# Performance work log

Hardware: AMD Instinct MI355X
Metric: run time of the kernel (lower is better)

The kernel has to match this reference:

```python
import jax, jax.numpy as jnp
import numpy as np

HIDDEN = 1024
HEADS = 16
HEAD_DIM = HIDDEN // HEADS


def setup_inputs() -> dict:
    key = jax.random.key(0)
    ks = jax.random.split(key, 9)
    s = 1.0 / np.sqrt(HIDDEN)
    inp = {
        "x": jax.random.normal(ks[0], (2, 2048, HIDDEN), dtype=jnp.float32),
        "Wq": jax.random.uniform(ks[1], (HIDDEN, HIDDEN), jnp.float32, -s, s),
        "bq": jax.random.uniform(ks[2], (HIDDEN,), jnp.float32, -s, s),
        "Wk": jax.random.uniform(ks[3], (HIDDEN, HIDDEN), jnp.float32, -s, s),
        "bk": jax.random.uniform(ks[4], (HIDDEN,), jnp.float32, -s, s),
        "Wv": jax.random.uniform(ks[5], (HIDDEN, HIDDEN), jnp.float32, -s, s),
        "bv": jax.random.uniform(ks[6], (HIDDEN,), jnp.float32, -s, s),
        "Wo": jax.random.uniform(ks[7], (HIDDEN, HIDDEN), jnp.float32, -s, s),
        "bo": jax.random.uniform(ks[8], (HIDDEN,), jnp.float32, -s, s),
    }
    return inp


def reference(x, Wq, bq, Wk, bk, Wv, bv, Wo, bo):
    B, S, _ = x.shape
    # QKV projections; reshape to [B, H, S, D]
    def heads(t):
        return t.reshape(B, S, HEADS, HEAD_DIM).transpose(0, 2, 1, 3)
    q = heads(x @ Wq + bq)
    k = heads(x @ Wk + bk)
    v = heads(x @ Wv + bv)
    scale = 1.0 / np.sqrt(HEAD_DIM)
    scores = jnp.einsum('bhqd,bhkd->bhqk', q, k) * scale  # [B,H,S,S]
    attn = jax.nn.softmax(scores, axis=-1)
    out = jnp.einsum('bhqk,bhkd->bhqd', attn, v)  # [B,H,S,D]
    out = out.transpose(0, 2, 1, 3).reshape(B, S, HIDDEN)
    return out @ Wo + bo
```

## Files before the change

kernel.cpp:

```cpp
#include <hip/hip_runtime.h>
#include <math.h>


namespace {

constexpr int kHID = 1024;
constexpr int kNH  = 16;
constexpr int kHD  = 64;
constexpr int kSEQ = 2048;

constexpr float kQScale = 0.125f * 1.4426950408889634f;

typedef unsigned short ushortT;
typedef __attribute__((ext_vector_type(8))) short   bf16x8;
typedef __attribute__((ext_vector_type(4))) float   f32x4;
typedef __attribute__((ext_vector_type(4))) unsigned short u16x4;

#define MFMA(a, b, c) __builtin_amdgcn_mfma_f32_16x16x32_bf16((a), (b), (c), 0, 0, 0)
#define SBAR() __builtin_amdgcn_s_barrier()
#define WAITV0() asm volatile("s_waitcnt vmcnt(0)" ::: "memory")
#define WAITV4() asm volatile("s_waitcnt vmcnt(4)" ::: "memory")
#define WAITV8() asm volatile("s_waitcnt vmcnt(8)" ::: "memory")

typedef const __attribute__((address_space(1))) void GVoid;
typedef __attribute__((address_space(3))) void SVoid;

__device__ __forceinline__ void gload_lds16(const ushortT* g, ushortT* l) {
    __builtin_amdgcn_global_load_lds((GVoid*)g, (SVoid*)l, 16, 0, 0);
}

__device__ __forceinline__ ushortT f2bf(float f) {
    unsigned u = __builtin_bit_cast(unsigned, f);
    u += 0x7fffu + ((u >> 16) & 1u);
    return (ushortT)(u >> 16);
}

__device__ __forceinline__ unsigned cvt_pk_bf16(float a, float b) {
    unsigned r;
    asm("v_cvt_pk_bf16_f32 %0, %1, %2" : "=v"(r) : "v"(a), "v"(b));
    return r;
}

__device__ __forceinline__ float4 ld4f(const float* p) { return *reinterpret_cast<const float4*>(p); }

__global__ __launch_bounds__(256) void cvtx_kernel(const float* __restrict__ x,
                                                   ushortT* __restrict__ xb) {
    const size_t i = ((size_t)blockIdx.x * 256 + threadIdx.x) * 4;
    const float4 f = ld4f(&x[i]);
    u16x4 o = { f2bf(f.x), f2bf(f.y), f2bf(f.z), f2bf(f.w) };
    *reinterpret_cast<u16x4*>(&xb[i]) = o;
}

__global__ __launch_bounds__(256) void transw_kernel(
    const float* __restrict__ W0, const float* __restrict__ W1,
    const float* __restrict__ W2, const float* __restrict__ W3,
    ushortT* __restrict__ WtAll) {
    __shared__ ushortT T[64 * 72];
    const float* W = (blockIdx.z == 0) ? W0 : (blockIdx.z == 1) ? W1 : (blockIdx.z == 2) ? W2 : W3;
    ushortT* Wt = WtAll + (size_t)blockIdx.z * kHID * kHID;
    const int kb = blockIdx.y * 64, nb = blockIdx.x * 64;
    const int tid = threadIdx.x;
    {
        const int kr = tid >> 2, nc = (tid & 3) * 16;
        #pragma unroll
        for (int i = 0; i < 16; i += 4) {
            const float4 f = ld4f(&W[(size_t)(kb + kr) * kHID + nb + nc + i]);
            T[kr * 72 + nc + i + 0] = f2bf(f.x);
            T[kr * 72 + nc + i + 1] = f2bf(f.y);
            T[kr * 72 + nc + i + 2] = f2bf(f.z);
            T[kr * 72 + nc + i + 3] = f2bf(f.w);
        }
    }
    __syncthreads();
    {
        const int nr = tid >> 2, kc = (tid & 3) * 16;
        ushortT tmp[16];
        #pragma unroll
        for (int i = 0; i < 16; ++i) tmp[i] = T[(kc + i) * 72 + nr];
        *reinterpret_cast<bf16x8*>(&Wt[(size_t)(nb + nr) * kHID + kb + kc]) =
            *reinterpret_cast<bf16x8*>(&tmp[0]);
        *reinterpret_cast<bf16x8*>(&Wt[(size_t)(nb + nr) * kHID + kb + kc + 8]) =
            *reinterpret_cast<bf16x8*>(&tmp[8]);
    }
}

template <typename Epi>
__device__ __forceinline__ void gemm128_body(
    const ushortT* __restrict__ A, const ushortT* __restrict__ Bt,
    int rowBase, int colBase, ushortT* As, ushortT* Bs, Epi&& epi) {
    const int tid = threadIdx.x, wid = tid >> 6, lane = tid & 63;
    const int hi = lane >> 4, lo = lane & 15;
    const int wr = wid >> 1, wc = wid & 1;
    const int r8 = lane >> 3, jc = lane & 7;

    const f32x4 z4 = {0.f, 0.f, 0.f, 0.f};
    f32x4 acc[4][4];
    #pragma unroll
    for (int mi = 0; mi < 4; ++mi)
        #pragma unroll
        for (int ni = 0; ni < 4; ++ni) acc[mi][ni] = z4;

    auto STAGE = [&](int buf, int k0) {
        #pragma unroll
        for (int i = 0; i < 4; ++i) {
            const int chunk = wid * 4 + i;
            const int row = chunk * 8 + r8;
            const int c8 = 8 * (jc ^ r8);
            gload_lds16(&A [(size_t)(rowBase + row) * kHID + k0 + c8], &As[buf * 8192 + chunk * 512]);
            gload_lds16(&Bt[(size_t)(colBase + row) * kHID + k0 + c8], &Bs[buf * 8192 + chunk * 512]);
        }
    };

    STAGE(0, 0);

    for (int t = 0; t < kHID / 64; ++t) {
        const int cur = t & 1;
        if (t + 1 < kHID / 64) {
            STAGE(cur ^ 1, (t + 1) * 64);
            WAITV8();
        } else {
            WAITV0();
        }
        SBAR();

        __builtin_amdgcn_s_setprio(1);
        #pragma unroll
        for (int ks = 0; ks < 2; ++ks) {
            bf16x8 af[4], bfr[4];
            #pragma unroll
            for (int mi = 0; mi < 4; ++mi) {
                const int row = 64 * wr + 16 * mi + lo;
                af[mi] = *reinterpret_cast<const bf16x8*>(
                    &As[cur * 8192 + row * 64 + 8 * ((4 * ks + hi) ^ (row & 7))]);
            }
            #pragma unroll
            for (int ni = 0; ni < 4; ++ni) {
                const int row = 64 * wc + 16 * ni + lo;
                bfr[ni] = *reinterpret_cast<const bf16x8*>(
                    &Bs[cur * 8192 + row * 64 + 8 * ((4 * ks + hi) ^ (row & 7))]);
            }
            #pragma unroll
            for (int mi = 0; mi < 4; ++mi)
                #pragma unroll
                for (int ni = 0; ni < 4; ++ni)
                    acc[mi][ni] = MFMA(af[mi], bfr[ni], acc[mi][ni]);
        }
        __builtin_amdgcn_s_setprio(0);

        SBAR();
    }

    epi(acc, wr, wc, hi, lo);
}

__global__ __launch_bounds__(256, 2) void qkv_mfma_gemm(
    const ushortT* __restrict__ A, const ushortT* __restrict__ WtAll,
    const float* __restrict__ bq, const float* __restrict__ bk, const float* __restrict__ bv,
    ushortT* __restrict__ qkvb) {
    __shared__ ushortT As[2 * 8192];
    __shared__ ushortT Bs[2 * 8192];

    const int z = blockIdx.z;
    const ushortT* Bt = WtAll + (size_t)z * kHID * kHID;
    const float* bias = (z == 0) ? bq : (z == 1) ? bk : bv;
    ushortT* out = qkvb + (size_t)z * 2 * kNH * kSEQ * kHD;
    const float scale = (z == 0) ? kQScale : 1.0f;
    const int rowBase = blockIdx.y * 128, colBase = blockIdx.x * 128;

    gemm128_body(A, Bt, rowBase, colBase, As, Bs,
        [&](f32x4 (&acc)[4][4], int wr, int wc, int hi, int lo) {
            #pragma unroll
            for (int ni = 0; ni < 4; ++ni) {
                const int col = colBase + 64 * wc + 16 * ni + lo;
                const float bcol = bias[col];
                const int h = col >> 6, d = col & 63;
                #pragma unroll
                for (int mi = 0; mi < 4; ++mi)
                    #pragma unroll
                    for (int r = 0; r < 4; ++r) {
                        const int m = rowBase + 64 * wr + 16 * mi + 4 * hi + r;
                        const int b = m >> 11, s = m & (kSEQ - 1);
                        const ushortT val = f2bf((acc[mi][ni][r] + bcol) * scale);
                        if (z == 2)
                            out[(((size_t)b * kNH + h) * kHD + d) * kSEQ + s] = val;
                        else
                            out[(((size_t)b * kNH + h) * kSEQ + s) * kHD + d] = val;
                    }
            }
        });
}

__global__ __launch_bounds__(256, 2) void out_mfma_gemm(
    const ushortT* __restrict__ A, const ushortT* __restrict__ Bt,
    const float* __restrict__ bias, float* __restrict__ out) {
    __shared__ ushortT As[2 * 8192];
    __shared__ ushortT Bs[2 * 8192];

    const int rowBase = blockIdx.y * 128, colBase = blockIdx.x * 128;

    gemm128_body(A, Bt, rowBase, colBase, As, Bs,
        [&](f32x4 (&acc)[4][4], int wr, int wc, int hi, int lo) {
            #pragma unroll
            for (int ni = 0; ni < 4; ++ni) {
                const int col = colBase + 64 * wc + 16 * ni + lo;
                const float bcol = bias[col];
                #pragma unroll
                for (int mi = 0; mi < 4; ++mi)
                    #pragma unroll
                    for (int r = 0; r < 4; ++r) {
                        const int m = rowBase + 64 * wr + 16 * mi + 4 * hi + r;
                        out[(size_t)m * kHID + col] = acc[mi][ni][r] + bcol;
                    }
            }
        });
}

__global__ __launch_bounds__(256, 4) void flash_mfma_kernel(
    const ushortT* __restrict__ Qb, const ushortT* __restrict__ Kb,
    const ushortT* __restrict__ Vtg, ushortT* __restrict__ Ob) {
    __shared__ ushortT Ks[2][64 * 64];
    __shared__ ushortT Vs[2][64 * 64];

    const int tid = threadIdx.x, wid = tid >> 6, lane = tid & 63;
    const int hi = lane >> 4, lo = lane & 15;
    const int h = blockIdx.x;
    const int q0 = blockIdx.y * 64;
    const size_t headBase = ((size_t)blockIdx.z * kNH + h) * (size_t)(kSEQ * kHD);
    const ushortT* Kg = Kb + headBase;
    const ushortT* Vg = Vtg + headBase;

    bf16x8 qf[2];
    #pragma unroll
    for (int c = 0; c < 2; ++c)
        qf[c] = *reinterpret_cast<const bf16x8*>(
            &Qb[headBase + (size_t)(q0 + 16 * wid + lo) * kHD + 32 * c + 8 * hi]);

    const short one = (short)0x3F80;
    const bf16x8 ones = {one, one, one, one, one, one, one, one};

    const f32x4 z4 = {0.f, 0.f, 0.f, 0.f};
    f32x4 acc[4] = {z4, z4, z4, z4};
    f32x4 accL = z4;

    const int r8 = lane >> 3, jc = lane & 7;

    const int kap0 = 8 * (lo >> 2) + (lo & 3);
    const int sk = (lo & 3) | (((lo >> 2) & 1) << 2);
    const int kx0 = (8 * hi) ^ (sk << 3);
    const int kx1 = (32 + 8 * hi) ^ (sk << 3);
    const int sv = (lo & 3) | (((lo >> 3) & 1) << 2);

    auto STAGE = [&](int buf, int kv0) {
        #pragma unroll
        for (int i = 0; i < 2; ++i) {
            const int rowBase = (i * 4 + wid) * 8;
            const int row = rowBase + r8;
            const int s8 = (r8 & 3) | ((wid & 1) << 2);
            gload_lds16(&Kg[(size_t)(kv0 + row) * kHD + 8 * (jc ^ s8)], &Ks[buf][rowBase * 64]);
            gload_lds16(&Vg[(size_t)row * kSEQ + kv0 + 8 * (jc ^ s8)], &Vs[buf][rowBase * 64]);
        }
    };

    STAGE(0, 0);

    for (int t = 0; t < kSEQ / 64; ++t) {
        const int cur = t & 1;
        if (t + 1 < kSEQ / 64) {
            STAGE(cur ^ 1, (t + 1) * 64);
            WAITV4();
        } else {
            WAITV0();
        }
        SBAR();

        f32x4 sc[4];
        __builtin_amdgcn_s_setprio(1);
        #pragma unroll
        for (int f = 0; f < 4; ++f) {
            const int kap = kap0 + 4 * (f & 1) + 32 * (f >> 1);
            const bf16x8 kf0 = *reinterpret_cast<const bf16x8*>(&Ks[cur][kap * 64 + kx0]);
            const bf16x8 kf1 = *reinterpret_cast<const bf16x8*>(&Ks[cur][kap * 64 + kx1]);
            sc[f] = MFMA(kf1, qf[1], MFMA(kf0, qf[0], z4));
        }
        __builtin_amdgcn_s_setprio(0);

        float p[4][4];
        #pragma unroll
        for (int f = 0; f < 4; ++f)
            #pragma unroll
            for (int r = 0; r < 4; ++r) p[f][r] = exp2f(sc[f][r]);

        union U { unsigned u[4]; bf16x8 v; };
        U pa0, pa1;
        pa0.u[0] = cvt_pk_bf16(p[0][0], p[0][1]);
        pa0.u[1] = cvt_pk_bf16(p[0][2], p[0][3]);
        pa0.u[2] = cvt_pk_bf16(p[1][0], p[1][1]);
        pa0.u[3] = cvt_pk_bf16(p[1][2], p[1][3]);
        pa1.u[0] = cvt_pk_bf16(p[2][0], p[2][1]);
        pa1.u[1] = cvt_pk_bf16(p[2][2], p[2][3]);
        pa1.u[2] = cvt_pk_bf16(p[3][0], p[3][1]);
        pa1.u[3] = cvt_pk_bf16(p[3][2], p[3][3]);

        __builtin_amdgcn_s_setprio(1);
        accL = MFMA(pa0.v, ones, accL);
        accL = MFMA(pa1.v, ones, accL);
        #pragma unroll
        for (int n = 0; n < 4; ++n) {
            const int vrow = 16 * n + lo;
            const bf16x8 vf0 = *reinterpret_cast<const bf16x8*>(
                &Vs[cur][vrow * 64 + ((8 * hi) ^ (sv << 3))]);
            const bf16x8 vf1 = *reinterpret_cast<const bf16x8*>(
                &Vs[cur][vrow * 64 + ((32 + 8 * hi) ^ (sv << 3))]);
            acc[n] = MFMA(pa0.v, vf0, acc[n]);
            acc[n] = MFMA(pa1.v, vf1, acc[n]);
        }
        __builtin_amdgcn_s_setprio(0);

        SBAR();
    }

    #pragma unroll
    for (int r = 0; r < 4; ++r) {
        const float inv = 1.0f / accL[r];
        const int s = q0 + 16 * wid + 4 * hi + r;
        const size_t base = ((size_t)blockIdx.z * kSEQ + s) * kHID + (size_t)h * kHD;
        #pragma unroll
        for (int n = 0; n < 4; ++n)
            Ob[base + 16 * n + lo] = f2bf(acc[n][r] * inv);
    }
}

}

extern "C" void kernel_launch(void* const* d_in, const int* in_sizes, int n_in,
                              void* d_out, int out_size, void* d_ws, size_t ws_size,
                              hipStream_t stream) {
    (void)in_sizes; (void)n_in; (void)out_size;
    const float* x  = (const float*)d_in[0];
    const float* Wq = (const float*)d_in[1];
    const float* bq = (const float*)d_in[2];
    const float* Wk = (const float*)d_in[3];
    const float* bk = (const float*)d_in[4];
    const float* Wv = (const float*)d_in[5];
    const float* bv = (const float*)d_in[6];
    const float* Wo = (const float*)d_in[7];
    const float* bo = (const float*)d_in[8];

    constexpr size_t kXE = (size_t)2 * kSEQ * kHID;
    constexpr size_t kWE = (size_t)kHID * kHID;
    const size_t needed = (kXE + 4 * kWE + 3 * kXE + kXE) * sizeof(ushortT);
    if (ws_size < needed) return;

    ushortT* xb    = (ushortT*)d_ws;
    ushortT* WtAll = xb + kXE;
    ushortT* qkvb  = WtAll + 4 * kWE;
    ushortT* attnb = qkvb + 3 * kXE;

    const ushortT* qb  = qkvb;
    const ushortT* kb  = qkvb + kXE;
    const ushortT* vtb = qkvb + 2 * kXE;

    cvtx_kernel<<<dim3((unsigned)(kXE / (256 * 4))), 256, 0, stream>>>(x, xb);
    transw_kernel<<<dim3(16, 16, 4), 256, 0, stream>>>(Wq, Wk, Wv, Wo, WtAll);

    qkv_mfma_gemm<<<dim3(8, 32, 3), 256, 0, stream>>>(xb, WtAll, bq, bk, bv, qkvb);

    flash_mfma_kernel<<<dim3(kNH, kSEQ / 64, 2), 256, 0, stream>>>(qb, kb, vtb, attnb);

    out_mfma_gemm<<<dim3(8, 32), 256, 0, stream>>>(attnb, WtAll + 3 * kWE, bo, (float*)d_out);
}
```

Baseline: 135.4 us.

## Halve GEMM K-tile, raise occupancy, shrink out-proj tile, merge prep kernels

Both GEMMs now stage K in 32-wide slices instead of 64, which halves LDS per block and lets the QKV GEMM declare four blocks per CU. The output projection switches to 64x128 tiles, doubling its grid so more CUs stay busy. The x conversion and weight transpose kernels are merged into one launch. The trade-off is twice as many barrier and wait iterations per GEMM and less reuse per staged tile.

```diff
diff --git a/kernel.cpp b/kernel.cpp
--- a/kernel.cpp
+++ b/kernel.cpp
@@ -19,8 +19,8 @@
 #define MFMA(a, b, c) __builtin_amdgcn_mfma_f32_16x16x32_bf16((a), (b), (c), 0, 0, 0)
 #define SBAR() __builtin_amdgcn_s_barrier()
 #define WAITV0() asm volatile("s_waitcnt vmcnt(0)" ::: "memory")
+#define WAITV3() asm volatile("s_waitcnt vmcnt(3)" ::: "memory")
 #define WAITV4() asm volatile("s_waitcnt vmcnt(4)" ::: "memory")
-#define WAITV8() asm volatile("s_waitcnt vmcnt(8)" ::: "memory")
 
 typedef const __attribute__((address_space(1))) void GVoid;
 typedef __attribute__((address_space(3))) void SVoid;
@@ -43,23 +43,28 @@
 
 __device__ __forceinline__ float4 ld4f(const float* p) { return *reinterpret_cast<const float4*>(p); }
 
-__global__ __launch_bounds__(256) void cvtx_kernel(const float* __restrict__ x,
-                                                   ushortT* __restrict__ xb) {
-    const size_t i = ((size_t)blockIdx.x * 256 + threadIdx.x) * 4;
-    const float4 f = ld4f(&x[i]);
-    u16x4 o = { f2bf(f.x), f2bf(f.y), f2bf(f.z), f2bf(f.w) };
-    *reinterpret_cast<u16x4*>(&xb[i]) = o;
-}
-
-__global__ __launch_bounds__(256) void transw_kernel(
+__global__ __launch_bounds__(256) void prep_kernel(
+    const float* __restrict__ x, ushortT* __restrict__ xb,
     const float* __restrict__ W0, const float* __restrict__ W1,
     const float* __restrict__ W2, const float* __restrict__ W3,
     ushortT* __restrict__ WtAll) {
     __shared__ ushortT T[64 * 72];
-    const float* W = (blockIdx.z == 0) ? W0 : (blockIdx.z == 1) ? W1 : (blockIdx.z == 2) ? W2 : W3;
-    ushortT* Wt = WtAll + (size_t)blockIdx.z * kHID * kHID;
-    const int kb = blockIdx.y * 64, nb = blockIdx.x * 64;
+    const int bx = blockIdx.x;
     const int tid = threadIdx.x;
+
+    if (bx < 4096) {
+        const size_t i = ((size_t)bx * 256 + tid) * 4;
+        const float4 f = ld4f(&x[i]);
+        u16x4 o = { f2bf(f.x), f2bf(f.y), f2bf(f.z), f2bf(f.w) };
+        *reinterpret_cast<u16x4*>(&xb[i]) = o;
+        return;
+    }
+
+    const int id2 = bx - 4096;
+    const int z = id2 >> 8;
+    const float* W = (z == 0) ? W0 : (z == 1) ? W1 : (z == 2) ? W2 : W3;
+    ushortT* Wt = WtAll + (size_t)z * kHID * kHID;
+    const int kb = ((id2 >> 4) & 15) * 64, nb = (id2 & 15) * 64;
     {
         const int kr = tid >> 2, nc = (tid & 3) * 16;
         #pragma unroll
@@ -84,135 +89,182 @@
     }
 }
 
-template <typename Epi>
-__device__ __forceinline__ void gemm128_body(
-    const ushortT* __restrict__ A, const ushortT* __restrict__ Bt,
-    int rowBase, int colBase, ushortT* As, ushortT* Bs, Epi&& epi) {
-    const int tid = threadIdx.x, wid = tid >> 6, lane = tid & 63;
-    const int hi = lane >> 4, lo = lane & 15;
-    const int wr = wid >> 1, wc = wid & 1;
-    const int r8 = lane >> 3, jc = lane & 7;
-
-    const f32x4 z4 = {0.f, 0.f, 0.f, 0.f};
-    f32x4 acc[4][4];
-    #pragma unroll
-    for (int mi = 0; mi < 4; ++mi)
-        #pragma unroll
-        for (int ni = 0; ni < 4; ++ni) acc[mi][ni] = z4;
-
-    auto STAGE = [&](int buf, int k0) {
-        #pragma unroll
-        for (int i = 0; i < 4; ++i) {
-            const int chunk = wid * 4 + i;
-            const int row = chunk * 8 + r8;
-            const int c8 = 8 * (jc ^ r8);
-            gload_lds16(&A [(size_t)(rowBase + row) * kHID + k0 + c8], &As[buf * 8192 + chunk * 512]);
-            gload_lds16(&Bt[(size_t)(colBase + row) * kHID + k0 + c8], &Bs[buf * 8192 + chunk * 512]);
-        }
-    };
-
-    STAGE(0, 0);
-
-    for (int t = 0; t < kHID / 64; ++t) {
-        const int cur = t & 1;
-        if (t + 1 < kHID / 64) {
-            STAGE(cur ^ 1, (t + 1) * 64);
-            WAITV8();
-        } else {
-            WAITV0();
-        }
-        SBAR();
-
-        __builtin_amdgcn_s_setprio(1);
-        #pragma unroll
-        for (int ks = 0; ks < 2; ++ks) {
-            bf16x8 af[4], bfr[4];
-            #pragma unroll
-            for (int mi = 0; mi < 4; ++mi) {
-                const int row = 64 * wr + 16 * mi + lo;
-                af[mi] = *reinterpret_cast<const bf16x8*>(
-                    &As[cur * 8192 + row * 64 + 8 * ((4 * ks + hi) ^ (row & 7))]);
-            }
-            #pragma unroll
-            for (int ni = 0; ni < 4; ++ni) {
-                const int row = 64 * wc + 16 * ni + lo;
-                bfr[ni] = *reinterpret_cast<const bf16x8*>(
-                    &Bs[cur * 8192 + row * 64 + 8 * ((4 * ks + hi) ^ (row & 7))]);
-            }
-            #pragma unroll
-            for (int mi = 0; mi < 4; ++mi)
-                #pragma unroll
-                for (int ni = 0; ni < 4; ++ni)
-                    acc[mi][ni] = MFMA(af[mi], bfr[ni], acc[mi][ni]);
-        }
-        __builtin_amdgcn_s_setprio(0);
-
-        SBAR();
-    }
-
-    epi(acc, wr, wc, hi, lo);
-}
-
-__global__ __launch_bounds__(256, 2) void qkv_mfma_gemm(
+__global__ __launch_bounds__(256, 4) void qkv_mfma_gemm(
     const ushortT* __restrict__ A, const ushortT* __restrict__ WtAll,
     const float* __restrict__ bq, const float* __restrict__ bk, const float* __restrict__ bv,
     ushortT* __restrict__ qkvb) {
-    __shared__ ushortT As[2 * 8192];
-    __shared__ ushortT Bs[2 * 8192];
+    __shared__ ushortT As[2 * 4096];
+    __shared__ ushortT Bs[2 * 4096];
 
     const int z = blockIdx.z;
     const ushortT* Bt = WtAll + (size_t)z * kHID * kHID;
     const float* bias = (z == 0) ? bq : (z == 1) ? bk : bv;
     ushortT* out = qkvb + (size_t)z * 2 * kNH * kSEQ * kHD;
     const float scale = (z == 0) ? kQScale : 1.0f;
+
+    const int tid = threadIdx.x, wid = tid >> 6, lane = tid & 63;
+    const int hi = lane >> 4, lo = lane & 15;
+    const int wr = wid >> 1, wc = wid & 1;
     const int rowBase = blockIdx.y * 128, colBase = blockIdx.x * 128;
-
-    gemm128_body(A, Bt, rowBase, colBase, As, Bs,
-        [&](f32x4 (&acc)[4][4], int wr, int wc, int hi, int lo) {
+    const int sr = lane >> 2, sj = lane & 3;
+
+    const f32x4 z4 = {0.f, 0.f, 0.f, 0.f};
+    f32x4 acc[4][4];
+    #pragma unroll
+    for (int mi = 0; mi < 4; ++mi)
+        #pragma unroll
+        for (int ni = 0; ni < 4; ++ni) acc[mi][ni] = z4;
+
+    auto STAGE = [&](int buf, int k0) {
+        #pragma unroll
+        for (int i = 0; i < 2; ++i) {
+            const int chunk = wid * 2 + i;
+            const int row = chunk * 16 + sr;
+            const int c8 = 8 * (sj ^ (sr & 3));
+            gload_lds16(&A [(size_t)(rowBase + row) * kHID + k0 + c8], &As[buf * 4096 + chunk * 512]);
+            gload_lds16(&Bt[(size_t)(colBase + row) * kHID + k0 + c8], &Bs[buf * 4096 + chunk * 512]);
+        }
+    };
+
+    STAGE(0, 0);
+
+    for (int t = 0; t < kHID / 32; ++t) {
+        const int cur = t & 1;
+        if (t + 1 < kHID / 32) {
+            STAGE(cur ^ 1, (t + 1) * 32);
+            WAITV4();
+        } else {
+            WAITV0();
+        }
+        SBAR();
+
+        __builtin_amdgcn_s_setprio(1);
+        bf16x8 af[4], bfr[4];
+        #pragma unroll
+        for (int mi = 0; mi < 4; ++mi) {
+            const int row = 64 * wr + 16 * mi + lo;
+            af[mi] = *reinterpret_cast<const bf16x8*>(
+                &As[cur * 4096 + row * 32 + 8 * (hi ^ (row & 3))]);
+        }
+        #pragma unroll
+        for (int ni = 0; ni < 4; ++ni) {
+            const int row = 64 * wc + 16 * ni + lo;
+            bfr[ni] = *reinterpret_cast<const bf16x8*>(
+                &Bs[cur * 4096 + row * 32 + 8 * (hi ^ (row & 3))]);
+        }
+        #pragma unroll
+        for (int mi = 0; mi < 4; ++mi)
             #pragma unroll
-            for (int ni = 0; ni < 4; ++ni) {
-                const int col = colBase + 64 * wc + 16 * ni + lo;
-                const float bcol = bias[col];
-                const int h = col >> 6, d = col & 63;
-                #pragma unroll
-                for (int mi = 0; mi < 4; ++mi)
-                    #pragma unroll
-                    for (int r = 0; r < 4; ++r) {
-                        const int m = rowBase + 64 * wr + 16 * mi + 4 * hi + r;
-                        const int b = m >> 11, s = m & (kSEQ - 1);
-                        const ushortT val = f2bf((acc[mi][ni][r] + bcol) * scale);
-                        if (z == 2)
-                            out[(((size_t)b * kNH + h) * kHD + d) * kSEQ + s] = val;
-                        else
-                            out[(((size_t)b * kNH + h) * kSEQ + s) * kHD + d] = val;
-                    }
+            for (int ni = 0; ni < 4; ++ni)
+                acc[mi][ni] = MFMA(af[mi], bfr[ni], acc[mi][ni]);
+        __builtin_amdgcn_s_setprio(0);
+
+        SBAR();
+    }
+
+    #pragma unroll
+    for (int ni = 0; ni < 4; ++ni) {
+        const int col = colBase + 64 * wc + 16 * ni + lo;
+        const float bcol = bias[col];
+        const int h = col >> 6, d = col & 63;
+        #pragma unroll
+        for (int mi = 0; mi < 4; ++mi)
+            #pragma unroll
+            for (int r = 0; r < 4; ++r) {
+                const int m = rowBase + 64 * wr + 16 * mi + 4 * hi + r;
+                const int b = m >> 11, s = m & (kSEQ - 1);
+                const ushortT val = f2bf((acc[mi][ni][r] + bcol) * scale);
+                if (z == 2)
+                    out[(((size_t)b * kNH + h) * kHD + d) * kSEQ + s] = val;
+                else
+                    out[(((size_t)b * kNH + h) * kSEQ + s) * kHD + d] = val;
             }
-        });
+    }
 }
 
 __global__ __launch_bounds__(256, 2) void out_mfma_gemm(
     const ushortT* __restrict__ A, const ushortT* __restrict__ Bt,
     const float* __restrict__ bias, float* __restrict__ out) {
-    __shared__ ushortT As[2 * 8192];
-    __shared__ ushortT Bs[2 * 8192];
-
-    const int rowBase = blockIdx.y * 128, colBase = blockIdx.x * 128;
-
-    gemm128_body(A, Bt, rowBase, colBase, As, Bs,
-        [&](f32x4 (&acc)[4][4], int wr, int wc, int hi, int lo) {
+    __shared__ ushortT As[2 * 2048];
+    __shared__ ushortT Bs[2 * 4096];
+
+    const int tid = threadIdx.x, wid = tid >> 6, lane = tid & 63;
+    const int hi = lane >> 4, lo = lane & 15;
+    const int wr = wid >> 1, wc = wid & 1;
+    const int rowBase = blockIdx.y * 64, colBase = blockIdx.x * 128;
+    const int sr = lane >> 2, sj = lane & 3;
+
+    const f32x4 z4 = {0.f, 0.f, 0.f, 0.f};
+    f32x4 acc[2][4];
+    #pragma unroll
+    for (int mi = 0; mi < 2; ++mi)
+        #pragma unroll
+        for (int ni = 0; ni < 4; ++ni) acc[mi][ni] = z4;
+
+    auto STAGE = [&](int buf, int k0) {
+        {
+            const int chunk = wid;
+            const int row = chunk * 16 + sr;
+            const int c8 = 8 * (sj ^ (sr & 3));
+            gload_lds16(&A[(size_t)(rowBase + row) * kHID + k0 + c8], &As[buf * 2048 + chunk * 512]);
+        }
+        #pragma unroll
+        for (int i = 0; i < 2; ++i) {
+            const int chunk = wid * 2 + i;
+            const int row = chunk * 16 + sr;
+            const int c8 = 8 * (sj ^ (sr & 3));
+            gload_lds16(&Bt[(size_t)(colBase + row) * kHID + k0 + c8], &Bs[buf * 4096 + chunk * 512]);
+        }
+    };
+
+    STAGE(0, 0);
+
+    for (int t = 0; t < kHID / 32; ++t) {
+        const int cur = t & 1;
+        if (t + 1 < kHID / 32) {
+            STAGE(cur ^ 1, (t + 1) * 32);
+            WAITV3();
+        } else {
+            WAITV0();
+        }
+        SBAR();
+
+        __builtin_amdgcn_s_setprio(1);
+        bf16x8 af[2], bfr[4];
+        #pragma unroll
+        for (int mi = 0; mi < 2; ++mi) {
+            const int row = 32 * wr + 16 * mi + lo;
+            af[mi] = *reinterpret_cast<const bf16x8*>(
+                &As[cur * 2048 + row * 32 + 8 * (hi ^ (row & 3))]);
+        }
+        #pragma unroll
+        for (int ni = 0; ni < 4; ++ni) {
+            const int row = 64 * wc + 16 * ni + lo;
+            bfr[ni] = *reinterpret_cast<const bf16x8*>(
+                &Bs[cur * 4096 + row * 32 + 8 * (hi ^ (row & 3))]);
+        }
+        #pragma unroll
+        for (int mi = 0; mi < 2; ++mi)
             #pragma unroll
-            for (int ni = 0; ni < 4; ++ni) {
-                const int col = colBase + 64 * wc + 16 * ni + lo;
-                const float bcol = bias[col];
-                #pragma unroll
-                for (int mi = 0; mi < 4; ++mi)
-                    #pragma unroll
-                    for (int r = 0; r < 4; ++r) {
-                        const int m = rowBase + 64 * wr + 16 * mi + 4 * hi + r;
-                        out[(size_t)m * kHID + col] = acc[mi][ni][r] + bcol;
-                    }
+            for (int ni = 0; ni < 4; ++ni)
+                acc[mi][ni] = MFMA(af[mi], bfr[ni], acc[mi][ni]);
+        __builtin_amdgcn_s_setprio(0);
+
+        SBAR();
+    }
+
+    #pragma unroll
+    for (int ni = 0; ni < 4; ++ni) {
+        const int col = colBase + 64 * wc + 16 * ni + lo;
+        const float bcol = bias[col];
+        #pragma unroll
+        for (int mi = 0; mi < 2; ++mi)
+            #pragma unroll
+            for (int r = 0; r < 4; ++r) {
+                const int m = rowBase + 32 * wr + 16 * mi + 4 * hi + r;
+                out[(size_t)m * kHID + col] = acc[mi][ni][r] + bcol;
             }
-        });
+    }
 }
 
 __global__ __launch_bounds__(256, 4) void flash_mfma_kernel(
@@ -360,12 +412,12 @@
     const ushortT* kb  = qkvb + kXE;
     const ushortT* vtb = qkvb + 2 * kXE;
 
-    cvtx_kernel<<<dim3((unsigned)(kXE / (256 * 4))), 256, 0, stream>>>(x, xb);
-    transw_kernel<<<dim3(16, 16, 4), 256, 0, stream>>>(Wq, Wk, Wv, Wo, WtAll);
+    prep_kernel<<<dim3(4096 + 4 * 256), 256, 0, stream>>>(
+        x, xb, Wq, Wk, Wv, Wo, WtAll);
 
     qkv_mfma_gemm<<<dim3(8, 32, 3), 256, 0, stream>>>(xb, WtAll, bq, bk, bv, qkvb);
 
     flash_mfma_kernel<<<dim3(kNH, kSEQ / 64, 2), 256, 0, stream>>>(qb, kb, vtb, attnb);
 
-    out_mfma_gemm<<<dim3(8, 32), 256, 0, stream>>>(attnb, WtAll + 3 * kWE, bo, (float*)d_out);
-}
+    out_mfma_gemm<<<dim3(8, 64), 256, 0, stream>>>(attnb, WtAll + 3 * kWE, bo, (float*)d_out);
+}
```

Result: faster. 126.8 us, median of 2 (-6.3%).
